# Kernel tuning notes

Hardware: AMD Instinct MI355X
Metric: run time of the kernel (lower is better)

Reference implementation:

```python
import jax, jax.numpy as jnp
import numpy as np

B = 64          # batch
NV = 256        # n_vert per rod
CS = [256, 256] # cs_n_vert
N = 3 * NV      # num_nodes
RBC = [100, 200]  # rigid_body_coupling_index
HID = 128


def _build_adjacency():
    A = np.zeros((N, N), dtype=np.float32)
    # chain edges: parent rod, child1 rod, child2 rod (hop=1)
    for i in range(NV - 1):
        A[i, i + 1] = 1; A[i + 1, i] = 1
    for i in range(NV, NV + CS[0] - 1):
        A[i, i + 1] = 1; A[i + 1, i] = 1
    for i in range(2 * NV, 2 * NV + CS[1] - 1):
        A[i, i + 1] = 1; A[i + 1, i] = 1
    zero_mask = np.all(A == 0, axis=-1).astype(np.float32)  # (N,)
    A = (A + np.eye(N, dtype=np.float32)) * (1.0 - zero_mask)  # broadcast over columns, as in torch
    # rigid-body coupling edges (asymmetric, faithful to the source)
    for i, r in enumerate(RBC):
        base = NV * (i + 1)
        A[base, r - 1] = 1; A[base, r] = 1; A[base, r + 1] = 1
        if i == 0:
            A[r, NV] = 1; A[r, NV + 1] = 1
        else:
            A[r, NV + CS[i - 1]] = 1; A[r, NV + CS[i - 1] + 1] = 1
    return A


def setup_inputs() -> dict:
    key = jax.random.key(0)
    ks = jax.random.split(key, 10)
    dims = [(6, 2 * HID), (2 * HID, HID), (HID, HID), (HID, 3)]  # gcn1..gcn4
    params = {}
    for li, (fi, fo) in enumerate(dims):
        params[f"W{li+1}"] = jax.random.normal(ks[li], (fo, fi), jnp.float32) / np.sqrt(fi)
        params[f"b{li+1}"] = jnp.zeros((fo,), jnp.float32)
    return {
        "x": jax.random.normal(ks[8], (B, N, 6), jnp.float32),
        "inputs": jax.random.normal(ks[9], (B, N, 3), jnp.float32),
        "adjacency": jnp.asarray(_build_adjacency()),
        **params,
        "parent_sel": jnp.array([0, NV - 1], jnp.int32),
        "child1_sel": jnp.array([NV - 1], jnp.int32),
        "child2_sel": jnp.array([NV - 1], jnp.int32),
    }


def _gcn(A_norm, x, W, b):
    # linear then symmetric-normalized dense aggregation
    return jnp.einsum('ij,bjf->bif', A_norm, x @ W.T + b)


def reference(x, inputs, adjacency, W1, b1, W2, b2, W3, b3, W4, b4,
              parent_sel, child1_sel, child2_sel):
    deg = adjacency.sum(axis=-1)
    deg_safe = jnp.where(deg == 0, 1.0, deg)
    d = jnp.where(deg == 0, 0.0, deg_safe ** -0.5)
    A_norm = adjacency * d[:, None] * d[None, :]

    x4 = x.reshape(B, 3, NV, -1)
    in4 = inputs.reshape(B, 3, NV, 3)
    # clamp input positions (first 3 features) at grasped vertices
    x4 = x4.at[:, 0, parent_sel, 0:3].set(in4[:, 0, parent_sel])
    x4 = x4.at[:, 1, child1_sel, 0:3].set(in4[:, 1, child1_sel])
    x4 = x4.at[:, 2, child2_sel, 0:3].set(in4[:, 2, child2_sel])
    h = x4.reshape(B, N, -1)

    h = jax.nn.relu(_gcn(A_norm, h, W1, b1))
    h = jax.nn.relu(_gcn(A_norm, h, W2, b2))
    h = _gcn(A_norm, h, W3, b3)
    out = _gcn(A_norm, h, W4, b4)

    o4 = out.reshape(B, 3, NV, 3)
    o4 = o4.at[:, 0, parent_sel].set(in4[:, 0, parent_sel])
    o4 = o4.at[:, 1, child1_sel].set(in4[:, 1, child1_sel])
    o4 = o4.at[:, 2, child2_sel].set(in4[:, 2, child2_sel])
    return o4.reshape(B, N, 3)
```

## Files before the change

### kernel.cpp

```cpp
#include <hip/hip_runtime.h>
#include <math.h>

#define B_ 64
#define NV_ 256
#define N_ 768
#define MAXNNZ 16
#define M_ (B_ * N_)

typedef unsigned short us8 __attribute__((ext_vector_type(8)));
typedef unsigned short us4 __attribute__((ext_vector_type(4)));
typedef __bf16 bf16x8 __attribute__((ext_vector_type(8)));
typedef float f32x4 __attribute__((ext_vector_type(4)));

__device__ inline float bf2f(unsigned short u) {
    return __uint_as_float(((unsigned int)u) << 16);
}
__device__ inline unsigned short f2bf(float f) {
    unsigned int u = __float_as_uint(f);
    unsigned int r = u + 0x7fffu + ((u >> 16) & 1u);
    return (unsigned short)(r >> 16);
}
__device__ inline bf16x8 ld_bf8(const unsigned short* p) {
    us8 u = *(const us8*)p;
    return __builtin_bit_cast(bf16x8, u);
}


__global__ __launch_bounds__(256) void k_deg_conv(
    const float* __restrict__ A, const float* __restrict__ W2,
    const float* __restrict__ W3, const int* __restrict__ psel, int np,
    const int* __restrict__ c1, int n1, const int* __restrict__ c2, int n2,
    float* __restrict__ dinv, int* __restrict__ clampf,
    unsigned short* __restrict__ W2b, unsigned short* __restrict__ W3b) {
    int blk = blockIdx.x, tid = threadIdx.x;
    if (blk < 192) {
        int wave = tid >> 6, lane = tid & 63;
        int i = blk * 4 + wave;
        float deg = 0.f;
#pragma unroll
        for (int c0 = 0; c0 < N_; c0 += 64) deg += A[(size_t)i * N_ + c0 + lane];
#pragma unroll
        for (int o = 32; o > 0; o >>= 1) deg += __shfl_xor(deg, o);
        if (lane == 0) dinv[i] = (deg == 0.f) ? 0.f : 1.0f / sqrtf(deg);
    } else if (blk < 384) {
        int idx = (blk - 192) * 256 + tid;
        if (idx < 128 * 256) W2b[idx] = f2bf(W2[idx]);
        else W3b[idx - 128 * 256] = f2bf(W3[idx - 128 * 256]);
    } else {
        clampf[tid] = 0;
        clampf[tid + 256] = 0;
        clampf[tid + 512] = 0;
        __syncthreads();
        if (tid < np) clampf[psel[tid]] = 1;
        else if (tid - np < n1) clampf[NV_ + c1[tid - np]] = 1;
        else if (tid - np - n1 < n2) clampf[2 * NV_ + c2[tid - np - n1]] = 1;
    }
}


__global__ __launch_bounds__(256) void k_sparse(const float* __restrict__ A,
                                                const float* __restrict__ dinv,
                                                int* __restrict__ cols,
                                                float* __restrict__ vals,
                                                int* __restrict__ nnzArr,
                                                float* __restrict__ rowsum) {
    int wave = threadIdx.x >> 6, lane = threadIdx.x & 63;
    int i = blockIdx.x * 4 + wave;
    float di = dinv[i];
    int cnt = 0;
    float rs = 0.f;
#pragma unroll
    for (int c0 = 0; c0 < N_; c0 += 64) {
        int c = c0 + lane;
        float a = A[(size_t)i * N_ + c];
        unsigned long long m = __ballot(a != 0.f);
        if (a != 0.f) {
            float v = a * di * dinv[c];
            int pos = cnt + __popcll(m & ((1ull << lane) - 1ull));
            if (pos < MAXNNZ) {
                cols[i * MAXNNZ + pos] = c;
                vals[i * MAXNNZ + pos] = v;
            }
            rs += v;
        }
        cnt += (int)__popcll(m);
    }
#pragma unroll
    for (int o = 32; o > 0; o >>= 1) rs += __shfl_xor(rs, o);
    if (lane == 0) {
        nnzArr[i] = cnt;
        rowsum[i] = rs;
    }
}


__global__ __launch_bounds__(256) void k_layer12(
    const float* __restrict__ x, const float* __restrict__ inputs,
    const int* __restrict__ cols, const float* __restrict__ vals,
    const int* __restrict__ nnzArr, const int* __restrict__ clampf,
    const float* __restrict__ rowsum, const float* __restrict__ W1,
    const float* __restrict__ b1, const unsigned short* __restrict__ W2b,
    const float* __restrict__ b2, unsigned short* __restrict__ T2) {
    __shared__ float Xs[64][6];
    __shared__ float W1T[6][256];
    __shared__ float b1s[256];

    int tid = threadIdx.x;
    int blk = ((blockIdx.x & 7) * 96) + (blockIdx.x >> 3);
    int i0 = (blk % 12) * 64;
    int base = (blk / 12) * N_;
    int wave = tid >> 6, lane = tid & 63;
    int lrow = lane & 15, kgrp = lane >> 4;

    for (int t = tid; t < 1536; t += 256) {
        int k = t >> 8, c = t & 255;
        W1T[k][c] = W1[c * 6 + k];
    }
    b1s[tid] = b1[tid];

    for (int t = lane; t < 96; t += 64) {
        int f = t % 6, ro = t / 6;
        int i = i0 + wave * 16 + ro;
        int n = nnzArr[i];
        if (n > MAXNNZ) n = MAXNNZ;
        float s = 0.f;
        for (int k = 0; k < n; ++k) {
            int c = cols[i * MAXNNZ + k];
            float val = (f < 3 && clampf[c]) ? inputs[(size_t)(base + c) * 3 + f]
                                             : x[(size_t)(base + c) * 6 + f];
            s += vals[i * MAXNNZ + k] * val;
        }
        Xs[wave * 16 + ro][f] = s;
    }
    __syncthreads();

    int i = i0 + wave * 16 + lrow;
    size_t g = (size_t)(base + i);
    float rs = rowsum[i];
    float xa[6];
#pragma unroll
    for (int k = 0; k < 6; ++k) xa[k] = Xs[wave * 16 + lrow][k];

    f32x4 acc[8];
#pragma unroll
    for (int j = 0; j < 8; ++j) acc[j] = (f32x4){0.f, 0.f, 0.f, 0.f};

#pragma unroll
    for (int s = 0; s < 8; ++s) {
        int c0 = s * 32 + kgrp * 8;
        float h[8];
        f32x4 bv0 = *(const f32x4*)&b1s[c0];
        f32x4 bv1 = *(const f32x4*)&b1s[c0 + 4];
#pragma unroll
        for (int e = 0; e < 4; ++e) {
            h[e] = rs * bv0[e];
            h[4 + e] = rs * bv1[e];
        }
#pragma unroll
        for (int k = 0; k < 6; ++k) {
            f32x4 w0 = *(const f32x4*)&W1T[k][c0];
            f32x4 w1 = *(const f32x4*)&W1T[k][c0 + 4];
#pragma unroll
            for (int e = 0; e < 4; ++e) {
                h[e] += xa[k] * w0[e];
                h[4 + e] += xa[k] * w1[e];
            }
        }
        us8 o;
#pragma unroll
        for (int e = 0; e < 8; ++e) o[e] = f2bf(fmaxf(h[e], 0.f));
        bf16x8 af = __builtin_bit_cast(bf16x8, o);
#pragma unroll
        for (int j = 0; j < 8; ++j) {
            bf16x8 w = ld_bf8(W2b + (size_t)(j * 16 + lrow) * 256 + c0);
            acc[j] = __builtin_amdgcn_mfma_f32_16x16x32_bf16(w, af, acc[j], 0, 0, 0);
        }
    }

#pragma unroll
    for (int j = 0; j < 8; ++j) {
        f32x4 bv = *(const f32x4*)&b2[j * 16 + kgrp * 4];
        us4 o;
#pragma unroll
        for (int e = 0; e < 4; ++e) o[e] = f2bf(acc[j][e] + bv[e]);
        *(us4*)(T2 + g * 128 + j * 16 + kgrp * 4) = o;
    }
}


__global__ __launch_bounds__(256) void k_layer3s(
    const unsigned short* __restrict__ T2, const int* __restrict__ cols,
    const float* __restrict__ vals, const int* __restrict__ nnzArr,
    const unsigned short* __restrict__ W3b, const float* __restrict__ b3,
    const float* __restrict__ W4, float* __restrict__ S) {
    __shared__ float W4s[128 * 3];

    int tid = threadIdx.x;
    int blk = ((blockIdx.x & 7) * 96) + (blockIdx.x >> 3);
    int i0 = (blk % 12) * 64;
    int base = (blk / 12) * N_;
    int wave = tid >> 6, lane = tid & 63;
    int lrow = lane & 15, kgrp = lane >> 4;

    for (int t = tid; t < 384; t += 256) {
        int d = t % 3, nfeat = t / 3;
        W4s[t] = W4[d * 128 + nfeat];
    }
    __syncthreads();

    int i = i0 + wave * 16 + lrow;
    size_t g = (size_t)(base + i);
    int n = nnzArr[i];
    if (n > MAXNNZ) n = MAXNNZ;

    float fa[4][8];
#pragma unroll
    for (int s = 0; s < 4; ++s)
#pragma unroll
        for (int e = 0; e < 8; ++e) fa[s][e] = 0.f;

    for (int k = 0; k < n; ++k) {
        int c = cols[i * MAXNNZ + k];
        float v = vals[i * MAXNNZ + k];
        const unsigned short* p = T2 + (size_t)(base + c) * 128 + kgrp * 8;
#pragma unroll
        for (int s = 0; s < 4; ++s) {
            us8 z = *(const us8*)(p + s * 32);
#pragma unroll
            for (int e = 0; e < 8; ++e) fa[s][e] += v * bf2f(z[e]);
        }
    }

    bf16x8 af[4];
#pragma unroll
    for (int s = 0; s < 4; ++s) {
        us8 o;
#pragma unroll
        for (int e = 0; e < 8; ++e) o[e] = f2bf(fmaxf(fa[s][e], 0.f));
        af[s] = __builtin_bit_cast(bf16x8, o);
    }

    f32x4 acc[8];
#pragma unroll
    for (int j = 0; j < 8; ++j) acc[j] = (f32x4){0.f, 0.f, 0.f, 0.f};
#pragma unroll
    for (int s = 0; s < 4; ++s) {
#pragma unroll
        for (int j = 0; j < 8; ++j) {
            bf16x8 w = ld_bf8(W3b + (size_t)(j * 16 + lrow) * 128 + s * 32 + kgrp * 8);
            acc[j] = __builtin_amdgcn_mfma_f32_16x16x32_bf16(w, af[s], acc[j], 0, 0, 0);
        }
    }

    float s0 = 0.f, s1 = 0.f, s2 = 0.f;
#pragma unroll
    for (int j = 0; j < 8; ++j) {
        f32x4 bv = *(const f32x4*)&b3[j * 16 + kgrp * 4];
#pragma unroll
        for (int e = 0; e < 4; ++e) {
            float tv = acc[j][e] + bv[e];
            int nfeat = j * 16 + kgrp * 4 + e;
            s0 += tv * W4s[nfeat * 3 + 0];
            s1 += tv * W4s[nfeat * 3 + 1];
            s2 += tv * W4s[nfeat * 3 + 2];
        }
    }
    s0 += __shfl_xor(s0, 16); s0 += __shfl_xor(s0, 32);
    s1 += __shfl_xor(s1, 16); s1 += __shfl_xor(s1, 32);
    s2 += __shfl_xor(s2, 16); s2 += __shfl_xor(s2, 32);
    if (kgrp == 0) {
        S[g * 3 + 0] = s0;
        S[g * 3 + 1] = s1;
        S[g * 3 + 2] = s2;
    }
}


__global__ __launch_bounds__(256) void k_out2(const float* __restrict__ S,
                                              const float* __restrict__ inputs,
                                              const int* __restrict__ cols,
                                              const float* __restrict__ vals,
                                              const int* __restrict__ nnzArr,
                                              const float* __restrict__ rowsum,
                                              const float* __restrict__ b4,
                                              const int* __restrict__ clampf,
                                              float* __restrict__ out) {
    int idx = blockIdx.x * 256 + threadIdx.x;
    if (idx >= M_ * 3) return;
    int f = idx % 3;
    int r = idx / 3;
    int i = r % N_;
    int base = r - i;
    if (clampf[i]) {
        out[idx] = inputs[(size_t)r * 3 + f];
        return;
    }
    int n = nnzArr[i];
    if (n > MAXNNZ) n = MAXNNZ;
    float s = rowsum[i] * b4[f];
    for (int k = 0; k < n; ++k) {
        int c = cols[i * MAXNNZ + k];
        int nc = nnzArr[c];
        if (nc > MAXNNZ) nc = MAXNNZ;
        float u = 0.f;
        for (int p = 0; p < nc; ++p) {
            int j = cols[c * MAXNNZ + p];
            u += vals[c * MAXNNZ + p] * S[(size_t)(base + j) * 3 + f];
        }
        s += vals[i * MAXNNZ + k] * u;
    }
    out[idx] = s;
}


extern "C" void kernel_launch(void* const* d_in, const int* in_sizes, int n_in,
                              void* d_out, int out_size, void* d_ws, size_t ws_size,
                              hipStream_t stream) {
    const float* x      = (const float*)d_in[0];
    const float* inputs = (const float*)d_in[1];
    const float* A      = (const float*)d_in[2];
    const float* W1     = (const float*)d_in[3];
    const float* b1     = (const float*)d_in[4];
    const float* W2     = (const float*)d_in[5];
    const float* b2     = (const float*)d_in[6];
    const float* W3     = (const float*)d_in[7];
    const float* b3     = (const float*)d_in[8];
    const float* W4     = (const float*)d_in[9];
    const float* b4     = (const float*)d_in[10];
    const int* psel     = (const int*)d_in[11];
    const int* c1sel    = (const int*)d_in[12];
    const int* c2sel    = (const int*)d_in[13];
    int np = in_sizes[11], n1 = in_sizes[12], n2 = in_sizes[13];
    float* out = (float*)d_out;

    char* ws = (char*)d_ws;
    float* dinv            = (float*)(ws + 0);
    float* rowsum          = (float*)(ws + 3072);
    int*   nnzA            = (int*)(ws + 6144);
    int*   clampf          = (int*)(ws + 9216);
    int*   cols            = (int*)(ws + 12288);
    float* vals            = (float*)(ws + 61440);
    unsigned short* W2b    = (unsigned short*)(ws + 110592);
    unsigned short* W3b    = (unsigned short*)(ws + 176128);
    float* S               = (float*)(ws + 417792);
    unsigned short* T2     = (unsigned short*)(ws + 27144192);

    k_deg_conv<<<385, 256, 0, stream>>>(A, W2, W3, psel, np, c1sel, n1, c2sel, n2,
                                        dinv, clampf, W2b, W3b);
    k_sparse<<<192, 256, 0, stream>>>(A, dinv, cols, vals, nnzA, rowsum);

    k_layer12<<<M_ / 64, 256, 0, stream>>>(x, inputs, cols, vals, nnzA, clampf, rowsum,
                                           W1, b1, W2b, b2, T2);
    k_layer3s<<<M_ / 64, 256, 0, stream>>>(T2, cols, vals, nnzA, W3b, b3, W4, S);
    k_out2<<<(M_ * 3 + 255) / 256, 256, 0, stream>>>(S, inputs, cols, vals, nnzA,
                                                     rowsum, b4, clampf, out);
}
```

Measured before the change: 74.24 us.

## Split two-hop output aggregation into two one-hop kernels and drop block swizzle

```diff
diff --git a/kernel.cpp b/kernel.cpp
--- a/kernel.cpp
+++ b/kernel.cpp
@@ -44,8 +44,8 @@
         if (lane == 0) dinv[i] = (deg == 0.f) ? 0.f : 1.0f / sqrtf(deg);
     } else if (blk < 384) {
         int idx = (blk - 192) * 256 + tid;
-        if (idx < 128 * 256) W2b[idx] = f2bf(W2[idx]);
-        else W3b[idx - 128 * 256] = f2bf(W3[idx - 128 * 256]);
+        if (idx < 32768) W2b[idx] = f2bf(W2[idx]);
+        else W3b[idx - 32768] = f2bf(W3[idx - 32768]);
     } else {
         clampf[tid] = 0;
         clampf[tid + 256] = 0;
@@ -106,7 +106,7 @@
     __shared__ float b1s[256];
 
     int tid = threadIdx.x;
-    int blk = ((blockIdx.x & 7) * 96) + (blockIdx.x >> 3);
+    int blk = blockIdx.x;
     int i0 = (blk % 12) * 64;
     int base = (blk / 12) * N_;
     int wave = tid >> 6, lane = tid & 63;
@@ -122,7 +122,6 @@
         int f = t % 6, ro = t / 6;
         int i = i0 + wave * 16 + ro;
         int n = nnzArr[i];
-        if (n > MAXNNZ) n = MAXNNZ;
         float s = 0.f;
         for (int k = 0; k < n; ++k) {
             int c = cols[i * MAXNNZ + k];
@@ -196,7 +195,7 @@
     __shared__ float W4s[128 * 3];
 
     int tid = threadIdx.x;
-    int blk = ((blockIdx.x & 7) * 96) + (blockIdx.x >> 3);
+    int blk = blockIdx.x;
     int i0 = (blk % 12) * 64;
     int base = (blk / 12) * N_;
     int wave = tid >> 6, lane = tid & 63;
@@ -276,15 +275,37 @@
 }
 
 
-__global__ __launch_bounds__(256) void k_out2(const float* __restrict__ S,
-                                              const float* __restrict__ inputs,
+__global__ __launch_bounds__(256) void k_aggS(const float* __restrict__ S,
                                               const int* __restrict__ cols,
                                               const float* __restrict__ vals,
                                               const int* __restrict__ nnzArr,
-                                              const float* __restrict__ rowsum,
-                                              const float* __restrict__ b4,
-                                              const int* __restrict__ clampf,
-                                              float* __restrict__ out) {
+                                              float* __restrict__ U) {
+    int idx = blockIdx.x * 256 + threadIdx.x;
+    if (idx >= M_ * 3) return;
+    int f = idx % 3;
+    int r = idx / 3;
+    int i = r % N_;
+    int base = r - i;
+    int n = nnzArr[i];
+    if (n > MAXNNZ) n = MAXNNZ;
+    float s = 0.f;
+    for (int k = 0; k < n; ++k) {
+        int c = cols[i * MAXNNZ + k];
+        s += vals[i * MAXNNZ + k] * S[(size_t)(base + c) * 3 + f];
+    }
+    U[idx] = s;
+}
+
+
+__global__ __launch_bounds__(256) void k_out(const float* __restrict__ U,
+                                             const float* __restrict__ inputs,
+                                             const int* __restrict__ cols,
+                                             const float* __restrict__ vals,
+                                             const int* __restrict__ nnzArr,
+                                             const float* __restrict__ rowsum,
+                                             const float* __restrict__ b4,
+                                             const int* __restrict__ clampf,
+                                             float* __restrict__ out) {
     int idx = blockIdx.x * 256 + threadIdx.x;
     if (idx >= M_ * 3) return;
     int f = idx % 3;
@@ -300,14 +321,7 @@
     float s = rowsum[i] * b4[f];
     for (int k = 0; k < n; ++k) {
         int c = cols[i * MAXNNZ + k];
-        int nc = nnzArr[c];
-        if (nc > MAXNNZ) nc = MAXNNZ;
-        float u = 0.f;
-        for (int p = 0; p < nc; ++p) {
-            int j = cols[c * MAXNNZ + p];
-            u += vals[c * MAXNNZ + p] * S[(size_t)(base + j) * 3 + f];
-        }
-        s += vals[i * MAXNNZ + k] * u;
+        s += vals[i * MAXNNZ + k] * U[(size_t)(base + c) * 3 + f];
     }
     out[idx] = s;
 }
@@ -343,6 +357,7 @@
     unsigned short* W2b    = (unsigned short*)(ws + 110592);
     unsigned short* W3b    = (unsigned short*)(ws + 176128);
     float* S               = (float*)(ws + 417792);
+    float* U               = (float*)(ws + 1048576);
     unsigned short* T2     = (unsigned short*)(ws + 27144192);
 
     k_deg_conv<<<385, 256, 0, stream>>>(A, W2, W3, psel, np, c1sel, n1, c2sel, n2,
@@ -352,6 +367,7 @@
     k_layer12<<<M_ / 64, 256, 0, stream>>>(x, inputs, cols, vals, nnzA, clampf, rowsum,
                                            W1, b1, W2b, b2, T2);
     k_layer3s<<<M_ / 64, 256, 0, stream>>>(T2, cols, vals, nnzA, W3b, b3, W4, S);
-    k_out2<<<(M_ * 3 + 255) / 256, 256, 0, stream>>>(S, inputs, cols, vals, nnzA,
-                                                     rowsum, b4, clampf, out);
-}
+    k_aggS<<<(M_ * 3 + 255) / 256, 256, 0, stream>>>(S, cols, vals, nnzA, U);
+    k_out<<<(M_ * 3 + 255) / 256, 256, 0, stream>>>(U, inputs, cols, vals, nnzA,
+                                                    rowsum, b4, clampf, out);
+}
```

Result: faster. 72.16 us (-2.8%).
